# Kernel optimization log

Measured on AMD Instinct MI355X. Metric: run time of the kernel, lower is better.

## Reference

```python
import jax, jax.numpy as jnp
import numpy as np

BLOCKS = 32
BLOCK_SIZE = 8
CONV_SHAPES = [(128, 96), (128, 128), (96, 128)] * 2  # per-block conv (out,in) list


def build_conv_meta():
    meta = []
    w_total = 0
    b_total = 0
    for _ in range(BLOCKS):
        for oc, ic in CONV_SHAPES:
            meta.append((oc, ic, w_total, b_total))
            w_total += oc * ic * 9
            b_total += oc
    return meta, w_total, b_total

CONV_META, W_TOTAL, B_TOTAL = build_conv_meta()


def build_program():
    ops = [[0, 0, 0, 0], [1, 0, 0, 0], [2, 0, 0, 0]]
    for blk in range(BLOCKS):
        ops.append([3, 0, 1, 2])  # SPLIT r0 -> (r1, r2)
        for rnd in range(2):
            ci = blk * 6 + rnd * 3
            ops += [
                [4, 3, 2, ci],      # r3 = conv(r2)        128<-96
                [5, 3, 3, 0],       # r3 = relu(r3)
                [4, 3, 3, ci + 1],  # r3 = conv(r3)        128<-128
                [5, 3, 3, 0],       # r3 = relu(r3)
                [4, 3, 3, ci + 2],  # r3 = conv(r3)        96<-128
                [6, 1, 1, 3],       # r1 = r1 + r3
                [9, 1, 2, 0],       # swap(r1, r2)  (Feistel)
            ]
        ops += [[7, 0, 1, 2],       # r0 = concat(r1, r2)
                [8, 0, 0, blk]]     # r0 = mix[blk] @ r0 (1x1 conv)
    return np.array(ops, dtype=np.int64)


def space_to_depth(x, blk):
    b, c, h, w = x.shape
    x = x.reshape(b, c, h // blk, blk, w // blk, blk)
    x = jnp.transpose(x, (0, 1, 3, 5, 2, 4))
    return x.reshape(b, c * blk * blk, h // blk, w // blk)


def conv3x3(x, w, b):
    y = jax.lax.conv_general_dilated(
        x, w, window_strides=(1, 1), padding=[(1, 1), (1, 1)],
        dimension_numbers=('NCHW', 'OIHW', 'NCHW'))
    return y + b[None, :, None, None]


def run_program(x, mu, sigma, w_flat, b_flat, m, perm, ops):
    regs = [x, None, None, None, None]
    for row in np.asarray(ops):
        op, a, b, c = (int(v) for v in row)
        if op == 0:  # AFFINE
            regs[a] = (regs[a] - mu[None, :, None, None]) / sigma[None, :, None, None]
        elif op == 1:  # PERM: gather along flattened HW per channel
            bs, ch, h, w = regs[a].shape
            v = regs[a].reshape(bs, ch, h * w)
            regs[a] = jnp.take_along_axis(v, perm[None], axis=2).reshape(bs, ch, h, w)
        elif op == 2:  # S2D
            regs[a] = space_to_depth(regs[a], BLOCK_SIZE)
        elif op == 3:  # SPLIT
            regs[b], regs[c] = jnp.split(regs[a], 2, axis=1)
        elif op == 4:  # CONV (weights sliced from flat buffer, static offsets)
            oc, ic, woff, boff = CONV_META[c]
            w = w_flat[woff:woff + oc * ic * 9].reshape(oc, ic, 3, 3)
            bb = b_flat[boff:boff + oc]
            regs[a] = conv3x3(regs[b], w, bb)
        elif op == 5:  # RELU
            regs[a] = jax.nn.relu(regs[b])
        elif op == 6:  # ADD
            regs[a] = regs[b] + regs[c]
        elif op == 7:  # CONCAT
            regs[a] = jnp.concatenate([regs[b], regs[c]], axis=1)
        elif op == 8:  # MIX: 1x1 conv with 192x192 orthogonal matrix
            regs[a] = jnp.einsum('oc,bchw->bohw', m[c], regs[b])
        elif op == 9:  # SWAP
            regs[a], regs[b] = regs[b], regs[a]
        else:
            raise ValueError('bad op')
    return regs[0]


def setup_inputs() -> dict:
    key = jax.random.key(0)
    k_x, k_w, k_b = jax.random.split(key, 3)
    rng = np.random.default_rng(0)

    x = jax.random.normal(k_x, (8, 3, 256, 256), dtype=jnp.float32)
    mu = jnp.full((3,), 0.45, dtype=jnp.float32)
    sigma = jnp.full((3,), 0.2, dtype=jnp.float32)
    # conv weights ~ He-ish scale so activations stay bounded across 64 Feistel rounds
    w_flat = jax.random.normal(k_w, (W_TOTAL,), dtype=jnp.float32) * 0.04
    b_flat = jax.random.normal(k_b, (B_TOTAL,), dtype=jnp.float32) * 0.01
    # orthogonal 192x192 mix matrices per block (as in nn.init.orthogonal_)
    ms = []
    for _ in range(BLOCKS):
        q, r = np.linalg.qr(rng.standard_normal((192, 192)))
        q = q * np.sign(np.diag(r))[None, :]
        ms.append(q.astype(np.float32))
    m = jnp.asarray(np.stack(ms))  # [BLOCKS,192,192]
    # per-channel spatial permutation on the 256x256 input
    perm = jnp.asarray(np.stack([rng.permutation(256 * 256) for _ in range(3)]).astype(np.int32))
    ops = build_program()  # static numpy tape
    return {'x': x, 'mu': mu, 'sigma': sigma, 'w_flat': w_flat, 'b_flat': b_flat,
            'm': m, 'perm': perm, 'ops': ops}


def reference(x, mu, sigma, w_flat, b_flat, m, perm, ops):
    return run_program(x, mu, sigma, w_flat, b_flat, m, perm, ops)
```

## Files before the change

### kernel.cpp

```cpp
#include <hip/hip_runtime.h>

typedef _Float16 f16;
typedef _Float16 f16x8 __attribute__((ext_vector_type(8)));
typedef _Float16 f16x4 __attribute__((ext_vector_type(4)));
typedef float    f32x4 __attribute__((ext_vector_type(4)));

#define GLOAD16(gp, lp) __builtin_amdgcn_global_load_lds(                      \
    (const __attribute__((address_space(1))) void*)(gp),                       \
    (__attribute__((address_space(3))) void*)(lp), 16, 0, 0)

__global__ __launch_bounds__(256) void prologue_k(
    const float* __restrict__ x, const float* __restrict__ mu,
    const float* __restrict__ sigma, const int* __restrict__ perm,
    f16* __restrict__ A0)
{
    int gid = blockIdx.x * 256 + threadIdx.x;
    if (gid >= 8192 * 24) return;
    int c8 = gid % 24;
    int p  = gid / 24;
    int b  = p >> 10;
    int h2 = (p >> 5) & 31;
    int w2 = p & 31;
    int cc = c8 >> 3;
    int bh = c8 & 7;
    const int* pm = &perm[cc * 65536 + (h2 * 8 + bh) * 256 + w2 * 8];
    const float* xp = &x[(b * 3 + cc) * 65536];
    float m = mu[cc], rs = 1.0f / sigma[cc];
    f16 v[8];
#pragma unroll
    for (int k = 0; k < 8; ++k)
        v[k] = (f16)((xp[pm[k]] - m) * rs);
    *(f16x8*)&A0[(size_t)p * 192 + c8 * 8] = *(f16x8*)v;
}

__global__ __launch_bounds__(256) void wconv_k(const float* __restrict__ wf,
                                               f16* __restrict__ wh)
{
    int c   = blockIdx.y;
    int s   = c % 6;
    int s3  = s % 3;
    int icr = (s3 == 0) ? 96 : 128;
    int ocv = (s3 == 2) ? 96 : 128;
    int nc8 = icr >> 3;
    int wo  = (s3 == 0 ? 0 : (s3 == 1 ? 110592 : 258048)) + (s >= 3 ? 368640 : 0);
    int idx = blockIdx.x * 256 + threadIdx.x;
    if (idx >= nc8 * ocv) return;
    int o  = idx % ocv;
    int c8 = idx / ocv;
    size_t base = (size_t)(c / 6) * 737280 + wo;
    const float* src = &wf[base + ((size_t)o * icr + c8 * 8) * 9];
    f16 vt[9][8];
#pragma unroll
    for (int k = 0; k < 8; ++k)
#pragma unroll
        for (int t = 0; t < 9; ++t)
            vt[t][k] = (f16)src[k * 9 + t];
#pragma unroll
    for (int t = 0; t < 9; ++t)
        *(f16x8*)&wh[base + ((size_t)(t * nc8 + c8) * ocv + o) * 8] = *(f16x8*)vt[t];
}

__global__ __launch_bounds__(256) void mconv_k(const float* __restrict__ mf,
                                               f16* __restrict__ mh)
{
    int n = blockIdx.x * 256 + threadIdx.x;
    if (n >= 32 * 24 * 192) return;
    int o   = n % 192;
    int t   = n / 192;
    int i8  = t % 24;
    int mat = t / 24;
    const float* s = &mf[(size_t)mat * 36864 + o * 192 + i8 * 8];
    f16 v[8];
#pragma unroll
    for (int k = 0; k < 8; ++k) v[k] = (f16)s[k];
    *(f16x8*)&mh[(size_t)mat * 36864 + ((size_t)i8 * 192 + o) * 8] = *(f16x8*)v;
}

__global__ __launch_bounds__(256) void bconv_k(const float* __restrict__ bf,
                                               float* __restrict__ bs, int n)
{
    int i = blockIdx.x * 256 + threadIdx.x;
    if (i < n) bs[i] = ldexpf(bf[i], -(i / 704));
}

template<int MMv, int OCV, int NC8R, int TAPS, bool RELU, bool ACCUM, bool OUT32>
__global__ __launch_bounds__(128) void conv_k(
    const f16* __restrict__ Xin, int ICS,
    const f16* __restrict__ W, const float* __restrict__ bias,
    f16* __restrict__ Out, int OCS, float* __restrict__ Out32, float scale)
{
    constexpr int PAD   = (TAPS == 9) ? 1 : 0;
    constexpr int ROWS  = 1 + 2 * PAD;
    constexpr int WW    = 32 + 2 * PAD;
    constexpr int NC8P  = (TAPS == 9) ? 16 : 32;
    constexpr int SWM   = NC8P - 1;
    constexpr int KC    = NC8R / 4;
    constexpr int OCW   = MMv * 16;
    constexpr int SLOTS = ROWS * WW * NC8P;

    __shared__ f16 xs[SLOTS * 8];

    const int tid  = threadIdx.x;
    const int lane = tid & 63, wave = tid >> 6;
    const int lq   = lane >> 4, ln = lane & 15;
    const int img  = blockIdx.x >> 5, row = blockIdx.x & 31;
    const int ocg  = blockIdx.y * (2 * OCW) + wave * OCW;

    for (int s0 = wave * 64; s0 < SLOTS; s0 += 128) {
        int s   = s0 + lane;
        int c8s = s & SWM;
        int wr  = s >> ((NC8P == 16) ? 4 : 5);
        int wv  = wr % WW;
        int ri  = wr / WW;
        int c8  = c8s ^ (wv & SWM);
        int r   = row - PAD + ri;
        int cl  = wv - PAD;
        bool live = (s < SLOTS) && (c8 < NC8R);
        bool inb  = ((unsigned)r < 32u) && ((unsigned)cl < 32u);
        if (live && inb) {
            GLOAD16(&Xin[(size_t)(img * 1024 + r * 32 + cl) * ICS + c8 * 8],
                    (char*)xs + (size_t)s0 * 16);
        } else if (live) {
            *(f16x8*)&xs[(size_t)s * 8] = (f16x8){};
        }
    }

    auto loadw = [&](f16x8 (&wr_)[KC][MMv], int tap) {
#pragma unroll
        for (int kc = 0; kc < KC; ++kc)
#pragma unroll
            for (int m = 0; m < MMv; ++m)
                wr_[kc][m] = *(const f16x8*)&W[
                    ((size_t)(tap * NC8R + kc * 4 + lq) * OCV + ocg + m * 16 + ln) * 8];
    };

    f16x8 w0[KC][MMv], w1[KC][MMv];
    loadw(w0, 0);

    asm volatile("s_waitcnt vmcnt(0) lgkmcnt(0)" ::: "memory");
    __syncthreads();

    f32x4 acc[MMv][2] = {};

#pragma unroll
    for (int tap = 0; tap < TAPS; ++tap) {
        const int dy = (TAPS == 9) ? tap / 3 - 1 : 0;
        const int dx = (TAPS == 9) ? tap % 3 - 1 : 0;
        if (tap + 1 < TAPS) {
            if (tap & 1) loadw(w0, tap + 1);
            else         loadw(w1, tap + 1);
        }
#pragma unroll
        for (int kc = 0; kc < KC; ++kc) {
            const int kcg = kc * 4 + lq;
            f16x8 b[2];
#pragma unroll
            for (int n = 0; n < 2; ++n) {
                int wv = n * 16 + ln + PAD + dx;
                b[n] = *(const f16x8*)&xs[
                    (size_t)(((PAD + dy) * WW + wv) * NC8P + (kcg ^ (wv & SWM))) * 8];
            }
#pragma unroll
            for (int m = 0; m < MMv; ++m) {
                const f16x8& a = (tap & 1) ? w1[kc][m] : w0[kc][m];
#pragma unroll
                for (int n = 0; n < 2; ++n)
                    acc[m][n] = __builtin_amdgcn_mfma_f32_16x16x32_f16(
                        a, b[n], acc[m][n], 0, 0, 0);
            }
        }
    }

#pragma unroll
    for (int m = 0; m < MMv; ++m) {
        const int oc = ocg + m * 16 + lq * 4;
        float b0 = 0.f, b1 = 0.f, b2 = 0.f, b3 = 0.f;
        if (TAPS == 9) {
            float4 bv = *(const float4*)&bias[oc];
            b0 = bv.x; b1 = bv.y; b2 = bv.z; b3 = bv.w;
        }
#pragma unroll
        for (int n = 0; n < 2; ++n) {
            float v0 = acc[m][n][0] * scale + b0;
            float v1 = acc[m][n][1] * scale + b1;
            float v2 = acc[m][n][2] * scale + b2;
            float v3 = acc[m][n][3] * scale + b3;
            if (RELU) {
                v0 = fmaxf(v0, 0.f); v1 = fmaxf(v1, 0.f);
                v2 = fmaxf(v2, 0.f); v3 = fmaxf(v3, 0.f);
            }
            if (OUT32) {
                size_t ob = (size_t)(img * 192 + oc) * 1024 + row * 32 + n * 16 + ln;
                Out32[ob]        = v0;
                Out32[ob + 1024] = v1;
                Out32[ob + 2048] = v2;
                Out32[ob + 3072] = v3;
            } else {
                const int p = img * 1024 + row * 32 + n * 16 + ln;
                f16* op = &Out[(size_t)p * OCS + oc];
                if (ACCUM) {
                    f16x4 old = *(const f16x4*)op;
                    v0 += (float)old[0]; v1 += (float)old[1];
                    v2 += (float)old[2]; v3 += (float)old[3];
                }
                f16x4 hv;
                hv[0] = (f16)v0; hv[1] = (f16)v1; hv[2] = (f16)v2; hv[3] = (f16)v3;
                *(f16x4*)op = hv;
            }
        }
    }
}

extern "C" void kernel_launch(void* const* d_in, const int* in_sizes, int n_in,
                              void* d_out, int out_size, void* d_ws, size_t ws_size,
                              hipStream_t stream)
{
    const float* x     = (const float*)d_in[0];
    const float* mu    = (const float*)d_in[1];
    const float* sigma = (const float*)d_in[2];
    const float* wf    = (const float*)d_in[3];
    const float* bf    = (const float*)d_in[4];
    const float* mf    = (const float*)d_in[5];
    const int*   perm  = (const int*)d_in[6];
    float*       out   = (float*)d_out;

    char* ws = (char*)d_ws;
    f16*   WH = (f16*)(ws);
    f16*   MH = (f16*)(ws + 47185920);
    float* BS = (float*)(ws + 49545216);
    f16*   XA = (f16*)(ws + 49635328);
    f16*   XB = (f16*)(ws + 52781056);
    f16*   H1 = (f16*)(ws + 55926784);
    f16*   H2 = (f16*)(ws + 58023936);

    wconv_k   <<<dim3(8, 192), 256, 0, stream>>>(wf, WH);
    mconv_k   <<<dim3(576),    256, 0, stream>>>(mf, MH);
    bconv_k   <<<dim3(88),     256, 0, stream>>>(bf, BS, 22528);
    prologue_k<<<dim3(768),    256, 0, stream>>>(x, mu, sigma, perm, XA);

    for (int blk = 0; blk < 32; ++blk) {
        size_t w0 = (size_t)blk * 737280;
        size_t b0 = (size_t)blk * 704;
        f16* cur = (blk & 1) ? XB : XA;
        f16* nxt = (blk & 1) ? XA : XB;
        conv_k<2, 128, 12, 9, true,  false, false><<<dim3(256, 2), 128, 0, stream>>>(
            cur + 96, 192, WH + w0 + 0,      BS + b0 + 0,   H1, 128, nullptr, 1.f);
        conv_k<2, 128, 16, 9, true,  false, false><<<dim3(256, 2), 128, 0, stream>>>(
            H1, 128,       WH + w0 + 110592, BS + b0 + 128, H2, 128, nullptr, 1.f);
        conv_k<3,  96, 16, 9, false, true,  false><<<dim3(256, 1), 128, 0, stream>>>(
            H2, 128,       WH + w0 + 258048, BS + b0 + 256, cur, 192, nullptr, 1.f);
        conv_k<2, 128, 12, 9, true,  false, false><<<dim3(256, 2), 128, 0, stream>>>(
            cur, 192,      WH + w0 + 368640, BS + b0 + 352, H1, 128, nullptr, 1.f);
        conv_k<2, 128, 16, 9, true,  false, false><<<dim3(256, 2), 128, 0, stream>>>(
            H1, 128,       WH + w0 + 479232, BS + b0 + 480, H2, 128, nullptr, 1.f);
        conv_k<3,  96, 16, 9, false, true,  false><<<dim3(256, 1), 128, 0, stream>>>(
            H2, 128,       WH + w0 + 626688, BS + b0 + 608, cur + 96, 192, nullptr, 1.f);
        if (blk < 31)
            conv_k<2, 192, 24, 1, false, false, false><<<dim3(256, 3), 128, 0, stream>>>(
                cur, 192, MH + (size_t)blk * 36864, nullptr, nxt, 192, nullptr, 0.5f);
        else
            conv_k<2, 192, 24, 1, false, false, true><<<dim3(256, 3), 128, 0, stream>>>(
                cur, 192, MH + (size_t)blk * 36864, nullptr, nullptr, 192, out,
                2147483648.f );
    }
}
```

Measured before the change: 2.782 ms.

## Fuse all conv layers into one persistent kernel with per-image barriers

Replaces the per-layer kernel launches with a single persistent kernel of 256 workgroups, each image handled by 32 workgroups that synchronize through an atomic-counter spin barrier between layers. Each workgroup now processes four output rows with a staged LDS tile and triple-buffered weight prefetch, and activations go through relaxed agent-scope atomic loads and stores for cross-workgroup visibility. This removes launch overhead and inter-kernel gaps, but relies on all workgroups being co-resident and replaces async global-to-LDS copies with register-staged loads.

```diff
diff --git a/kernel.cpp b/kernel.cpp
--- a/kernel.cpp
+++ b/kernel.cpp
@@ -4,10 +4,7 @@
 typedef _Float16 f16x8 __attribute__((ext_vector_type(8)));
 typedef _Float16 f16x4 __attribute__((ext_vector_type(4)));
 typedef float    f32x4 __attribute__((ext_vector_type(4)));
-
-#define GLOAD16(gp, lp) __builtin_amdgcn_global_load_lds(                      \
-    (const __attribute__((address_space(1))) void*)(gp),                       \
-    (__attribute__((address_space(3))) void*)(lp), 16, 0, 0)
+typedef unsigned long long u64;
 
 __global__ __launch_bounds__(256) void prologue_k(
     const float* __restrict__ x, const float* __restrict__ mu,
@@ -83,94 +80,124 @@
     if (i < n) bs[i] = ldexpf(bf[i], -(i / 704));
 }
 
+__device__ __forceinline__ f16x8 ld_act16(const f16* p)
+{
+    u64* q = (u64*)p;
+    union { u64 u[2]; f16x8 v; } c;
+    c.u[0] = __hip_atomic_load(q,     __ATOMIC_RELAXED, __HIP_MEMORY_SCOPE_AGENT);
+    c.u[1] = __hip_atomic_load(q + 1, __ATOMIC_RELAXED, __HIP_MEMORY_SCOPE_AGENT);
+    return c.v;
+}
+__device__ __forceinline__ f16x4 ld_act8(const f16* p)
+{
+    union { u64 u; f16x4 v; } c;
+    c.u = __hip_atomic_load((u64*)p, __ATOMIC_RELAXED, __HIP_MEMORY_SCOPE_AGENT);
+    return c.v;
+}
+__device__ __forceinline__ void st_act8(f16* p, f16x4 v)
+{
+    union { u64 u; f16x4 v; } c;
+    c.v = v;
+    __hip_atomic_store((u64*)p, c.u, __ATOMIC_RELAXED, __HIP_MEMORY_SCOPE_AGENT);
+}
+
+__device__ __forceinline__ void img_barrier(unsigned* ctr, unsigned target)
+{
+    asm volatile("s_waitcnt vmcnt(0) lgkmcnt(0)" ::: "memory");
+    __syncthreads();
+    if (threadIdx.x == 0) {
+        __hip_atomic_fetch_add(ctr, 1u, __ATOMIC_RELAXED, __HIP_MEMORY_SCOPE_AGENT);
+        while (__hip_atomic_load(ctr, __ATOMIC_RELAXED, __HIP_MEMORY_SCOPE_AGENT) < target)
+            __builtin_amdgcn_s_sleep(4);
+    }
+    __syncthreads();
+}
+
 template<int MMv, int OCV, int NC8R, int TAPS, bool RELU, bool ACCUM, bool OUT32>
-__global__ __launch_bounds__(128) void conv_k(
+__device__ __forceinline__ void layer(char* lds, int img, int local,
     const f16* __restrict__ Xin, int ICS,
     const f16* __restrict__ W, const float* __restrict__ bias,
     f16* __restrict__ Out, int OCS, float* __restrict__ Out32, float scale)
 {
-    constexpr int PAD   = (TAPS == 9) ? 1 : 0;
-    constexpr int ROWS  = 1 + 2 * PAD;
-    constexpr int WW    = 32 + 2 * PAD;
-    constexpr int NC8P  = (TAPS == 9) ? 16 : 32;
-    constexpr int SWM   = NC8P - 1;
-    constexpr int KC    = NC8R / 4;
-    constexpr int OCW   = MMv * 16;
-    constexpr int SLOTS = ROWS * WW * NC8P;
-
-    __shared__ f16 xs[SLOTS * 8];
-
-    const int tid  = threadIdx.x;
+    constexpr int OCW  = MMv * 16;
+    constexpr int NG   = OCV / OCW;
+    constexpr int PAD  = (TAPS == 9) ? 1 : 0;
+    constexpr int ROWS = 4 + 2 * PAD;
+    constexpr int WW   = 32 + 2 * PAD;
+    constexpr int NC8P = (NC8R + 7) & ~7;
+    constexpr int KC   = NC8R / 4;
+    constexpr int S    = ROWS * WW * NC8P;
+
+    const int tid   = threadIdx.x;
+    const int ocidx = local & 3;
+    if (ocidx >= NG) return;
+    const int rowg = local >> 2;
+    const int r0   = rowg * 4;
     const int lane = tid & 63, wave = tid >> 6;
     const int lq   = lane >> 4, ln = lane & 15;
-    const int img  = blockIdx.x >> 5, row = blockIdx.x & 31;
-    const int ocg  = blockIdx.y * (2 * OCW) + wave * OCW;
-
-    for (int s0 = wave * 64; s0 < SLOTS; s0 += 128) {
-        int s   = s0 + lane;
-        int c8s = s & SWM;
-        int wr  = s >> ((NC8P == 16) ? 4 : 5);
-        int wv  = wr % WW;
-        int ri  = wr / WW;
-        int c8  = c8s ^ (wv & SWM);
-        int r   = row - PAD + ri;
-        int cl  = wv - PAD;
-        bool live = (s < SLOTS) && (c8 < NC8R);
-        bool inb  = ((unsigned)r < 32u) && ((unsigned)cl < 32u);
-        if (live && inb) {
-            GLOAD16(&Xin[(size_t)(img * 1024 + r * 32 + cl) * ICS + c8 * 8],
-                    (char*)xs + (size_t)s0 * 16);
-        } else if (live) {
-            *(f16x8*)&xs[(size_t)s * 8] = (f16x8){};
-        }
-    }
-
-    auto loadw = [&](f16x8 (&wr_)[KC][MMv], int tap) {
+    const int ocg  = ocidx * OCW;
+
+    auto loadw = [&](f16x8 (&dst)[KC][MMv], int tap) {
 #pragma unroll
         for (int kc = 0; kc < KC; ++kc)
 #pragma unroll
             for (int m = 0; m < MMv; ++m)
-                wr_[kc][m] = *(const f16x8*)&W[
+                dst[kc][m] = *(const f16x8*)&W[
                     ((size_t)(tap * NC8R + kc * 4 + lq) * OCV + ocg + m * 16 + ln) * 8];
     };
-
-    f16x8 w0[KC][MMv], w1[KC][MMv];
+    f16x8 w0[KC][MMv], w1[KC][MMv], w2[KC][MMv];
     loadw(w0, 0);
-
-    asm volatile("s_waitcnt vmcnt(0) lgkmcnt(0)" ::: "memory");
+    if (TAPS > 1) loadw(w1, 1);
+
+    for (int s = tid; s < S; s += 256) {
+        int gslot = s % NC8P;
+        int rem   = s / NC8P;
+        int wv    = rem % WW;
+        int ri    = rem / WW;
+        int g     = (gslot & ~7) | ((gslot & 7) ^ (wv & 7));
+        if (g >= NC8R) continue;
+        int r  = r0 - PAD + ri;
+        int cl = wv - PAD;
+        f16x8 val = {};
+        if ((unsigned)r < 32u && (unsigned)cl < 32u)
+            val = ld_act16(&Xin[(size_t)(img * 1024 + r * 32 + cl) * ICS + g * 8]);
+        *(f16x8*)&lds[(size_t)s * 16] = val;
+    }
     __syncthreads();
 
     f32x4 acc[MMv][2] = {};
-
 #pragma unroll
     for (int tap = 0; tap < TAPS; ++tap) {
+        if (TAPS > 1 && tap + 2 < TAPS) {
+            if ((tap + 2) % 3 == 0)      loadw(w0, tap + 2);
+            else if ((tap + 2) % 3 == 1) loadw(w1, tap + 2);
+            else                         loadw(w2, tap + 2);
+        }
+        const f16x8 (&wt)[KC][MMv] =
+            (tap % 3 == 0) ? w0 : (tap % 3 == 1) ? w1 : w2;
         const int dy = (TAPS == 9) ? tap / 3 - 1 : 0;
         const int dx = (TAPS == 9) ? tap % 3 - 1 : 0;
-        if (tap + 1 < TAPS) {
-            if (tap & 1) loadw(w0, tap + 1);
-            else         loadw(w1, tap + 1);
-        }
+        const int ri = wave + PAD + dy;
 #pragma unroll
         for (int kc = 0; kc < KC; ++kc) {
             const int kcg = kc * 4 + lq;
             f16x8 b[2];
 #pragma unroll
             for (int n = 0; n < 2; ++n) {
-                int wv = n * 16 + ln + PAD + dx;
-                b[n] = *(const f16x8*)&xs[
-                    (size_t)(((PAD + dy) * WW + wv) * NC8P + (kcg ^ (wv & SWM))) * 8];
+                int wv    = n * 16 + ln + PAD + dx;
+                int gslot = (kcg & ~7) | ((kcg & 7) ^ (wv & 7));
+                b[n] = *(const f16x8*)&lds[(size_t)((ri * WW + wv) * NC8P + gslot) * 16];
             }
 #pragma unroll
-            for (int m = 0; m < MMv; ++m) {
-                const f16x8& a = (tap & 1) ? w1[kc][m] : w0[kc][m];
+            for (int m = 0; m < MMv; ++m)
 #pragma unroll
                 for (int n = 0; n < 2; ++n)
                     acc[m][n] = __builtin_amdgcn_mfma_f32_16x16x32_f16(
-                        a, b[n], acc[m][n], 0, 0, 0);
-            }
+                        wt[kc][m], b[n], acc[m][n], 0, 0, 0);
         }
     }
 
+    const int prow = r0 + wave;
 #pragma unroll
     for (int m = 0; m < MMv; ++m) {
         const int oc = ocg + m * 16 + lq * 4;
@@ -190,24 +217,72 @@
                 v2 = fmaxf(v2, 0.f); v3 = fmaxf(v3, 0.f);
             }
             if (OUT32) {
-                size_t ob = (size_t)(img * 192 + oc) * 1024 + row * 32 + n * 16 + ln;
+                size_t ob = (size_t)(img * 192 + oc) * 1024 + prow * 32 + n * 16 + ln;
                 Out32[ob]        = v0;
                 Out32[ob + 1024] = v1;
                 Out32[ob + 2048] = v2;
                 Out32[ob + 3072] = v3;
             } else {
-                const int p = img * 1024 + row * 32 + n * 16 + ln;
+                const int p = img * 1024 + prow * 32 + n * 16 + ln;
                 f16* op = &Out[(size_t)p * OCS + oc];
                 if (ACCUM) {
-                    f16x4 old = *(const f16x4*)op;
+                    f16x4 old = ld_act8(op);
                     v0 += (float)old[0]; v1 += (float)old[1];
                     v2 += (float)old[2]; v3 += (float)old[3];
                 }
                 f16x4 hv;
                 hv[0] = (f16)v0; hv[1] = (f16)v1; hv[2] = (f16)v2; hv[3] = (f16)v3;
-                *(f16x4*)op = hv;
+                st_act8(op, hv);
             }
         }
+    }
+}
+
+__global__ __launch_bounds__(256) void persist_k(
+    const f16* __restrict__ WH, const f16* __restrict__ MH,
+    const float* __restrict__ BS, f16* __restrict__ XA, f16* __restrict__ XB,
+    f16* __restrict__ H1, f16* __restrict__ H2, float* __restrict__ out,
+    unsigned* __restrict__ bar)
+{
+    __shared__ __align__(16) char lds[52224];
+    const int wg    = blockIdx.x;
+    const int img   = wg >> 5;
+    const int local = wg & 31;
+    unsigned* ctr = &bar[img * 16];
+    unsigned gen = 0;
+
+    for (int blk = 0; blk < 32; ++blk) {
+        const size_t w0 = (size_t)blk * 737280;
+        const size_t b0 = (size_t)blk * 704;
+        f16* cur = (blk & 1) ? XB : XA;
+        f16* nxt = (blk & 1) ? XA : XB;
+
+        layer<2, 128, 12, 9, true, false, false>(lds, img, local, cur + 96, 192,
+            WH + w0 + 0,      BS + b0 + 0,   H1, 128, nullptr, 1.f);
+        img_barrier(ctr, ++gen * 32u);
+        layer<2, 128, 16, 9, true, false, false>(lds, img, local, H1, 128,
+            WH + w0 + 110592, BS + b0 + 128, H2, 128, nullptr, 1.f);
+        img_barrier(ctr, ++gen * 32u);
+        layer<2, 96, 16, 9, false, true, false>(lds, img, local, H2, 128,
+            WH + w0 + 258048, BS + b0 + 256, cur, 192, nullptr, 1.f);
+        img_barrier(ctr, ++gen * 32u);
+        layer<2, 128, 12, 9, true, false, false>(lds, img, local, cur, 192,
+            WH + w0 + 368640, BS + b0 + 352, H1, 128, nullptr, 1.f);
+        img_barrier(ctr, ++gen * 32u);
+        layer<2, 128, 16, 9, true, false, false>(lds, img, local, H1, 128,
+            WH + w0 + 479232, BS + b0 + 480, H2, 128, nullptr, 1.f);
+        img_barrier(ctr, ++gen * 32u);
+        layer<2, 96, 16, 9, false, true, false>(lds, img, local, H2, 128,
+            WH + w0 + 626688, BS + b0 + 608, cur + 96, 192, nullptr, 1.f);
+        img_barrier(ctr, ++gen * 32u);
+        if (blk < 31)
+            layer<3, 192, 24, 1, false, false, false>(lds, img, local, cur, 192,
+                MH + (size_t)blk * 36864, nullptr, nxt, 192, nullptr, 0.5f);
+        else
+            layer<3, 192, 24, 1, false, false, true>(lds, img, local, cur, 192,
+                MH + (size_t)blk * 36864, nullptr, nullptr, 192, out,
+                2147483648.f );
+        img_barrier(ctr, ++gen * 32u);
     }
 }
 
@@ -225,42 +300,21 @@
     float*       out   = (float*)d_out;
 
     char* ws = (char*)d_ws;
-    f16*   WH = (f16*)(ws);
-    f16*   MH = (f16*)(ws + 47185920);
-    float* BS = (float*)(ws + 49545216);
-    f16*   XA = (f16*)(ws + 49635328);
-    f16*   XB = (f16*)(ws + 52781056);
-    f16*   H1 = (f16*)(ws + 55926784);
-    f16*   H2 = (f16*)(ws + 58023936);
+    f16*      WH  = (f16*)(ws);
+    f16*      MH  = (f16*)(ws + 47185920);
+    float*    BS  = (float*)(ws + 49545216);
+    f16*      XA  = (f16*)(ws + 49635328);
+    f16*      XB  = (f16*)(ws + 52781056);
+    f16*      H1  = (f16*)(ws + 55926784);
+    f16*      H2  = (f16*)(ws + 58023936);
+    unsigned* BAR = (unsigned*)(ws + 60121088);
+
+    hipMemsetAsync(BAR, 0, 4096, stream);
 
     wconv_k   <<<dim3(8, 192), 256, 0, stream>>>(wf, WH);
     mconv_k   <<<dim3(576),    256, 0, stream>>>(mf, MH);
     bconv_k   <<<dim3(88),     256, 0, stream>>>(bf, BS, 22528);
     prologue_k<<<dim3(768),    256, 0, stream>>>(x, mu, sigma, perm, XA);
 
-    for (int blk = 0; blk < 32; ++blk) {
-        size_t w0 = (size_t)blk * 737280;
-        size_t b0 = (size_t)blk * 704;
-        f16* cur = (blk & 1) ? XB : XA;
-        f16* nxt = (blk & 1) ? XA : XB;
-        conv_k<2, 128, 12, 9, true,  false, false><<<dim3(256, 2), 128, 0, stream>>>(
-            cur + 96, 192, WH + w0 + 0,      BS + b0 + 0,   H1, 128, nullptr, 1.f);
-        conv_k<2, 128, 16, 9, true,  false, false><<<dim3(256, 2), 128, 0, stream>>>(
-            H1, 128,       WH + w0 + 110592, BS + b0 + 128, H2, 128, nullptr, 1.f);
-        conv_k<3,  96, 16, 9, false, true,  false><<<dim3(256, 1), 128, 0, stream>>>(
-            H2, 128,       WH + w0 + 258048, BS + b0 + 256, cur, 192, nullptr, 1.f);
-        conv_k<2, 128, 12, 9, true,  false, false><<<dim3(256, 2), 128, 0, stream>>>(
-            cur, 192,      WH + w0 + 368640, BS + b0 + 352, H1, 128, nullptr, 1.f);
-        conv_k<2, 128, 16, 9, true,  false, false><<<dim3(256, 2), 128, 0, stream>>>(
-            H1, 128,       WH + w0 + 479232, BS + b0 + 480, H2, 128, nullptr, 1.f);
-        conv_k<3,  96, 16, 9, false, true,  false><<<dim3(256, 1), 128, 0, stream>>>(
-            H2, 128,       WH + w0 + 626688, BS + b0 + 608, cur + 96, 192, nullptr, 1.f);
-        if (blk < 31)
-            conv_k<2, 192, 24, 1, false, false, false><<<dim3(256, 3), 128, 0, stream>>>(
-                cur, 192, MH + (size_t)blk * 36864, nullptr, nxt, 192, nullptr, 0.5f);
-        else
-            conv_k<2, 192, 24, 1, false, false, true><<<dim3(256, 3), 128, 0, stream>>>(
-                cur, 192, MH + (size_t)blk * 36864, nullptr, nullptr, 192, out,
-                2147483648.f );
-    }
-}
+    persist_k<<<dim3(256), 256, 0, stream>>>(WH, MH, BS, XA, XB, H1, H2, out, BAR);
+}
```

Measured after the change: 3.362 ms. 20.8% more time.
